# Performance work log

Hardware: AMD Instinct MI355X
Metric: run time of the kernel (lower is better)

Reference implementation:

```python
import jax, jax.numpy as jnp
import numpy as np

N = 50000
K = 4
D_IN = 256
D_OUT = 64
E = 800000

def setup_inputs() -> dict:
    key = jax.random.key(0)
    k1, k2, k3, k4, k5 = jax.random.split(key, 5)
    x = jax.random.normal(k1, (N, K, D_IN), dtype=jnp.float32)
    weight = jax.random.normal(k2, (D_IN, D_OUT), dtype=jnp.float32) * (1.0 / np.sqrt(D_IN))
    adj_rows = jax.random.randint(k3, (E,), 0, N, dtype=jnp.int32)
    adj_cols = jax.random.randint(k4, (E,), 0, N, dtype=jnp.int32)
    adj_vals = jax.random.uniform(k5, (E,), dtype=jnp.float32)
    return {"x": x, "weight": weight, "adj_rows": adj_rows, "adj_cols": adj_cols, "adj_vals": adj_vals}

def reference(x, weight, adj_rows, adj_cols, adj_vals):
    # x: [N, K, D_in]; weight: [D_in, D_out]
    # dropout p=0.0 / eval mode -> identity
    # support = x @ W for every sample k, vectorized over K
    support = jnp.einsum('nkd,df->nkf', x, weight)          # [N, K, D_out]
    # sparse adj matmul: out[r] += vals[e] * support[cols[e]]
    msgs = adj_vals[:, None, None] * support[adj_cols]       # [E, K, D_out]
    out = jax.ops.segment_sum(msgs, adj_rows, num_segments=N)  # [N, K, D_out]
    return jax.nn.relu(out)
```

## Files before the change

kernel.cpp:

```cpp
#include <hip/hip_runtime.h>
#include <hip/hip_bf16.h>
#include <stdint.h>

#define D_IN   256
#define D_OUT  64
#define KHEADS 4
#define ROWLEN 256
#define GBM    128
#define LDAB   72
#define LDWB   72
#define CAP    128

typedef __attribute__((ext_vector_type(8))) short bf16x8;
typedef __attribute__((ext_vector_type(4))) float f32x4;

__device__ __forceinline__ unsigned short f2bf(float f) {
  unsigned u = __float_as_uint(f);
  return (unsigned short)((u + 0x7fffu + ((u >> 16) & 1u)) >> 16);
}

__global__ __launch_bounds__(256) void gemm_mfma(const float* __restrict__ X,
                                                 const float* __restrict__ W,
                                                 signed char* __restrict__ Sq,
                                                 float* __restrict__ scaleArr,
                                                 int M, int Nnodes) {
  __shared__ unsigned short lA[GBM * LDAB];
  __shared__ unsigned short lWt[64 * LDWB];
  const int t    = threadIdx.x;
  const int wave = t >> 6;
  const int lane = t & 63;
  const int q    = lane >> 4;
  const int l16  = lane & 15;
  const long row0 = (long)blockIdx.x * GBM;

  f32x4 acc[2][4];
#pragma unroll
  for (int rb = 0; rb < 2; ++rb)
#pragma unroll
    for (int cb = 0; cb < 4; ++cb) acc[rb][cb] = (f32x4){0.f, 0.f, 0.f, 0.f};

  for (int k0 = 0; k0 < D_IN; k0 += 64) {
#pragma unroll
    for (int j = 0; j < 8; ++j) {
      int flat = t + j * 256;
      int r    = flat >> 4;
      int kk   = (flat & 15) << 2;
      long gr  = row0 + r;
      if (gr >= M) gr = M - 1;
      float4 v = *(const float4*)&X[gr * D_IN + k0 + kk];
      ushort4 o;
      o.x = f2bf(v.x); o.y = f2bf(v.y); o.z = f2bf(v.z); o.w = f2bf(v.w);
      *(ushort4*)&lA[r * LDAB + kk] = o;
    }
#pragma unroll
    for (int j = 0; j < 4; ++j) {
      int flat = t + j * 256;
      int kr   = flat >> 4;
      int nn   = (flat & 15) << 2;
      float4 v = *(const float4*)&W[(size_t)(k0 + kr) * D_OUT + nn];
      lWt[(nn + 0) * LDWB + kr] = f2bf(v.x);
      lWt[(nn + 1) * LDWB + kr] = f2bf(v.y);
      lWt[(nn + 2) * LDWB + kr] = f2bf(v.z);
      lWt[(nn + 3) * LDWB + kr] = f2bf(v.w);
    }
    __syncthreads();

#pragma unroll
    for (int s = 0; s < 2; ++s) {
      bf16x8 a0 = *(const bf16x8*)&lA[(wave * 32 + 0  + l16) * LDAB + s * 32 + q * 8];
      bf16x8 a1 = *(const bf16x8*)&lA[(wave * 32 + 16 + l16) * LDAB + s * 32 + q * 8];
#pragma unroll
      for (int cb = 0; cb < 4; ++cb) {
        bf16x8 b = *(const bf16x8*)&lWt[(cb * 16 + l16) * LDWB + s * 32 + q * 8];
        acc[0][cb] = __builtin_amdgcn_mfma_f32_16x16x32_bf16(a0, b, acc[0][cb], 0, 0, 0);
        acc[1][cb] = __builtin_amdgcn_mfma_f32_16x16x32_bf16(a1, b, acc[1][cb], 0, 0, 0);
      }
    }
    __syncthreads();
  }

  float nm0 = 0.f, nm1 = 0.f;
#pragma unroll
  for (int cb = 0; cb < 4; ++cb)
#pragma unroll
    for (int reg = 0; reg < 4; ++reg) {
      nm0 = fmaxf(nm0, fabsf(acc[0][cb][reg]));
      nm1 = fmaxf(nm1, fabsf(acc[1][cb][reg]));
    }
#pragma unroll
  for (int d = 1; d < 16; d <<= 1) {
    nm0 = fmaxf(nm0, __shfl_xor(nm0, d, 64));
    nm1 = fmaxf(nm1, __shfl_xor(nm1, d, 64));
  }
  const float inv0 = (nm0 > 0.f) ? 127.f / nm0 : 0.f;
  const float inv1 = (nm1 > 0.f) ? 127.f / nm1 : 0.f;
  const int node_base = blockIdx.x * 32 + wave * 8;
  if (l16 == 0) {
    int n0 = node_base + q;
    int n1 = node_base + 4 + q;
    if (n0 < Nnodes) scaleArr[n0] = nm0 / 127.f;
    if (n1 < Nnodes) scaleArr[n1] = nm1 / 127.f;
  }
#pragma unroll
  for (int rb = 0; rb < 2; ++rb) {
    const float inv = rb ? inv1 : inv0;
#pragma unroll
    for (int cb = 0; cb < 4; ++cb)
#pragma unroll
      for (int reg = 0; reg < 4; ++reg) {
        long r = row0 + wave * 32 + rb * 16 + q * 4 + reg;
        if (r < M) {
          int qi = (int)rintf(acc[rb][cb][reg] * inv);
          Sq[r * D_OUT + cb * 16 + l16] = (signed char)qi;
        }
      }
  }
}

__global__ __launch_bounds__(256) void place_kernel(const int* __restrict__ rows,
                                                    const int* __restrict__ cols,
                                                    const float* __restrict__ vals,
                                                    const float* __restrict__ scaleArr,
                                                    int* __restrict__ cnt,
                                                    uint2* __restrict__ ecv, int E) {
  int e = blockIdx.x * 256 + threadIdx.x;
  if (e < E) {
    int r = rows[e];
    int c = cols[e];
    float vp = vals[e] * scaleArr[c];
    int pos = atomicAdd(&cnt[r], 1);
    if (pos < CAP)
      ecv[((size_t)r << 7) + pos] = make_uint2((unsigned)c, __float_as_uint(vp));
  }
}

__global__ __launch_bounds__(256) void gather_kernel(const int* __restrict__ Sqi,
                                                     const int* __restrict__ cnt,
                                                     const uint2* __restrict__ ecv,
                                                     float* __restrict__ out, int n) {
  const int lane = threadIdx.x & 63;
  const int r = blockIdx.x * 4 + (threadIdx.x >> 6);
  if (r >= n) return;
  int deg = cnt[r];
  if (deg > CAP) deg = CAP;
  const uint2* __restrict__ bucket = ecv + ((size_t)r << 7);

  float4 a0 = make_float4(0.f, 0.f, 0.f, 0.f);
  float4 a1 = a0, a2 = a0, a3 = a0;
  int i = 0;
  for (; i + 4 <= deg; i += 4) {
    uint2 c0 = bucket[i], c1 = bucket[i + 1], c2 = bucket[i + 2], c3 = bucket[i + 3];
    int w0 = Sqi[(size_t)c0.x * 64 + lane];
    int w1 = Sqi[(size_t)c1.x * 64 + lane];
    int w2 = Sqi[(size_t)c2.x * 64 + lane];
    int w3 = Sqi[(size_t)c3.x * 64 + lane];
    float v0 = __uint_as_float(c0.y), v1 = __uint_as_float(c1.y);
    float v2 = __uint_as_float(c2.y), v3 = __uint_as_float(c3.y);
    a0.x += v0 * (float)(w0 << 24 >> 24); a0.y += v0 * (float)(w0 << 16 >> 24);
    a0.z += v0 * (float)(w0 <<  8 >> 24); a0.w += v0 * (float)(w0 >> 24);
    a1.x += v1 * (float)(w1 << 24 >> 24); a1.y += v1 * (float)(w1 << 16 >> 24);
    a1.z += v1 * (float)(w1 <<  8 >> 24); a1.w += v1 * (float)(w1 >> 24);
    a2.x += v2 * (float)(w2 << 24 >> 24); a2.y += v2 * (float)(w2 << 16 >> 24);
    a2.z += v2 * (float)(w2 <<  8 >> 24); a2.w += v2 * (float)(w2 >> 24);
    a3.x += v3 * (float)(w3 << 24 >> 24); a3.y += v3 * (float)(w3 << 16 >> 24);
    a3.z += v3 * (float)(w3 <<  8 >> 24); a3.w += v3 * (float)(w3 >> 24);
  }
  for (; i < deg; ++i) {
    uint2 c0 = bucket[i];
    int w0 = Sqi[(size_t)c0.x * 64 + lane];
    float v0 = __uint_as_float(c0.y);
    a0.x += v0 * (float)(w0 << 24 >> 24); a0.y += v0 * (float)(w0 << 16 >> 24);
    a0.z += v0 * (float)(w0 <<  8 >> 24); a0.w += v0 * (float)(w0 >> 24);
  }
  float4 res;
  res.x = fmaxf(a0.x + a1.x + a2.x + a3.x, 0.f);
  res.y = fmaxf(a0.y + a1.y + a2.y + a3.y, 0.f);
  res.z = fmaxf(a0.z + a1.z + a2.z + a3.z, 0.f);
  res.w = fmaxf(a0.w + a1.w + a2.w + a3.w, 0.f);
  *(float4*)&out[(size_t)r * ROWLEN + (lane << 2)] = res;
}

extern "C" void kernel_launch(void* const* d_in, const int* in_sizes, int n_in,
                              void* d_out, int out_size, void* d_ws, size_t ws_size,
                              hipStream_t stream) {
  const float* x    = (const float*)d_in[0];
  const float* w    = (const float*)d_in[1];
  const int*   rows = (const int*)d_in[2];
  const int*   cols = (const int*)d_in[3];
  const float* vals = (const float*)d_in[4];
  float* out = (float*)d_out;

  const int E = in_sizes[2];
  const int N = in_sizes[0] / (KHEADS * D_IN);
  const int M = N * KHEADS;

  char* ws = (char*)d_ws;
  size_t o = 0;
  signed char* Sq = (signed char*)(ws + o); o += (size_t)M * D_OUT;
  o = (o + 15) & ~(size_t)15;
  float* scaleArr = (float*)(ws + o); o += (size_t)N * sizeof(float);
  o = (o + 15) & ~(size_t)15;
  int* cnt = (int*)(ws + o); o += (size_t)N * sizeof(int);
  o = (o + 15) & ~(size_t)15;
  uint2* ecv = (uint2*)(ws + o);

  hipMemsetAsync(cnt, 0, (size_t)N * sizeof(int), stream);

  gemm_mfma<<<(M + GBM - 1) / GBM, 256, 0, stream>>>(x, w, Sq, scaleArr, M, N);
  place_kernel<<<(E + 255) / 256, 256, 0, stream>>>(rows, cols, vals, scaleArr, cnt, ecv, E);
  gather_kernel<<<(N + 3) / 4, 256, 0, stream>>>((const int*)Sq, cnt, ecv, out, N);
}
```

Measured before the change: 397.0 us.

## Load A fragments directly from global in GEMM and widen gather unroll

The GEMM now stages all of W into shared memory once and has each lane load its A fragments straight from global memory into registers, converting to bf16 on the fly and prefetching the next k-slice. This removes the A tile in shared memory and the per-k-step barriers. The gather kernel processes edges in groups of 8 with clamped indices and zeroed weights for the tail, which raises the number of independent loads in flight. The trade-offs are global A loads that are less coalesced (each lane reads 32 contiguous bytes from a different row) and some redundant tail loads.

```diff
diff --git a/kernel.cpp b/kernel.cpp
--- a/kernel.cpp
+++ b/kernel.cpp
@@ -7,8 +7,7 @@
 #define KHEADS 4
 #define ROWLEN 256
 #define GBM    128
-#define LDAB   72
-#define LDWB   72
+#define LDWT   264
 #define CAP    128
 
 typedef __attribute__((ext_vector_type(8))) short bf16x8;
@@ -17,6 +16,17 @@
 __device__ __forceinline__ unsigned short f2bf(float f) {
   unsigned u = __float_as_uint(f);
   return (unsigned short)((u + 0x7fffu + ((u >> 16) & 1u)) >> 16);
+}
+
+__device__ __forceinline__ bf16x8 load_a_frag(const float* __restrict__ p) {
+  float4 u = *(const float4*)p;
+  float4 v = *(const float4*)(p + 4);
+  bf16x8 r;
+  r[0] = (short)f2bf(u.x); r[1] = (short)f2bf(u.y);
+  r[2] = (short)f2bf(u.z); r[3] = (short)f2bf(u.w);
+  r[4] = (short)f2bf(v.x); r[5] = (short)f2bf(v.y);
+  r[6] = (short)f2bf(v.z); r[7] = (short)f2bf(v.w);
+  return r;
 }
 
 __global__ __launch_bounds__(256) void gemm_mfma(const float* __restrict__ X,
@@ -24,8 +34,7 @@
                                                  signed char* __restrict__ Sq,
                                                  float* __restrict__ scaleArr,
                                                  int M, int Nnodes) {
-  __shared__ unsigned short lA[GBM * LDAB];
-  __shared__ unsigned short lWt[64 * LDWB];
+  __shared__ unsigned short lWt[64 * LDWT];
   const int t    = threadIdx.x;
   const int wave = t >> 6;
   const int lane = t & 63;
@@ -33,50 +42,48 @@
   const int l16  = lane & 15;
   const long row0 = (long)blockIdx.x * GBM;
 
+#pragma unroll
+  for (int j = 0; j < 16; ++j) {
+    int flat = t + j * 256;
+    int kr   = flat >> 4;
+    int nn   = (flat & 15) << 2;
+    float4 v = *(const float4*)&W[(size_t)kr * D_OUT + nn];
+    lWt[(nn + 0) * LDWT + kr] = f2bf(v.x);
+    lWt[(nn + 1) * LDWT + kr] = f2bf(v.y);
+    lWt[(nn + 2) * LDWT + kr] = f2bf(v.z);
+    lWt[(nn + 3) * LDWT + kr] = f2bf(v.w);
+  }
+  __syncthreads();
+
+  long r0 = row0 + wave * 32 + l16;
+  long r1 = r0 + 16;
+  if (r0 >= M) r0 = M - 1;
+  if (r1 >= M) r1 = M - 1;
+  const float* px0 = X + r0 * D_IN + q * 8;
+  const float* px1 = X + r1 * D_IN + q * 8;
+
   f32x4 acc[2][4];
 #pragma unroll
   for (int rb = 0; rb < 2; ++rb)
 #pragma unroll
     for (int cb = 0; cb < 4; ++cb) acc[rb][cb] = (f32x4){0.f, 0.f, 0.f, 0.f};
 
-  for (int k0 = 0; k0 < D_IN; k0 += 64) {
-#pragma unroll
-    for (int j = 0; j < 8; ++j) {
-      int flat = t + j * 256;
-      int r    = flat >> 4;
-      int kk   = (flat & 15) << 2;
-      long gr  = row0 + r;
-      if (gr >= M) gr = M - 1;
-      float4 v = *(const float4*)&X[gr * D_IN + k0 + kk];
-      ushort4 o;
-      o.x = f2bf(v.x); o.y = f2bf(v.y); o.z = f2bf(v.z); o.w = f2bf(v.w);
-      *(ushort4*)&lA[r * LDAB + kk] = o;
-    }
-#pragma unroll
-    for (int j = 0; j < 4; ++j) {
-      int flat = t + j * 256;
-      int kr   = flat >> 4;
-      int nn   = (flat & 15) << 2;
-      float4 v = *(const float4*)&W[(size_t)(k0 + kr) * D_OUT + nn];
-      lWt[(nn + 0) * LDWB + kr] = f2bf(v.x);
-      lWt[(nn + 1) * LDWB + kr] = f2bf(v.y);
-      lWt[(nn + 2) * LDWB + kr] = f2bf(v.z);
-      lWt[(nn + 3) * LDWB + kr] = f2bf(v.w);
-    }
-    __syncthreads();
-
-#pragma unroll
-    for (int s = 0; s < 2; ++s) {
-      bf16x8 a0 = *(const bf16x8*)&lA[(wave * 32 + 0  + l16) * LDAB + s * 32 + q * 8];
-      bf16x8 a1 = *(const bf16x8*)&lA[(wave * 32 + 16 + l16) * LDAB + s * 32 + q * 8];
-#pragma unroll
-      for (int cb = 0; cb < 4; ++cb) {
-        bf16x8 b = *(const bf16x8*)&lWt[(cb * 16 + l16) * LDWB + s * 32 + q * 8];
-        acc[0][cb] = __builtin_amdgcn_mfma_f32_16x16x32_bf16(a0, b, acc[0][cb], 0, 0, 0);
-        acc[1][cb] = __builtin_amdgcn_mfma_f32_16x16x32_bf16(a1, b, acc[1][cb], 0, 0, 0);
-      }
-    }
-    __syncthreads();
+  bf16x8 a0 = load_a_frag(px0);
+  bf16x8 a1 = load_a_frag(px1);
+#pragma unroll
+  for (int s = 0; s < 8; ++s) {
+    bf16x8 na0, na1;
+    if (s < 7) {
+      na0 = load_a_frag(px0 + (s + 1) * 32);
+      na1 = load_a_frag(px1 + (s + 1) * 32);
+    }
+#pragma unroll
+    for (int cb = 0; cb < 4; ++cb) {
+      bf16x8 b = *(const bf16x8*)&lWt[(cb * 16 + l16) * LDWT + s * 32 + q * 8];
+      acc[0][cb] = __builtin_amdgcn_mfma_f32_16x16x32_bf16(a0, b, acc[0][cb], 0, 0, 0);
+      acc[1][cb] = __builtin_amdgcn_mfma_f32_16x16x32_bf16(a1, b, acc[1][cb], 0, 0, 0);
+    }
+    a0 = na0; a1 = na1;
   }
 
   float nm0 = 0.f, nm1 = 0.f;
@@ -145,38 +152,41 @@
   if (deg > CAP) deg = CAP;
   const uint2* __restrict__ bucket = ecv + ((size_t)r << 7);
 
-  float4 a0 = make_float4(0.f, 0.f, 0.f, 0.f);
-  float4 a1 = a0, a2 = a0, a3 = a0;
-  int i = 0;
-  for (; i + 4 <= deg; i += 4) {
-    uint2 c0 = bucket[i], c1 = bucket[i + 1], c2 = bucket[i + 2], c3 = bucket[i + 3];
-    int w0 = Sqi[(size_t)c0.x * 64 + lane];
-    int w1 = Sqi[(size_t)c1.x * 64 + lane];
-    int w2 = Sqi[(size_t)c2.x * 64 + lane];
-    int w3 = Sqi[(size_t)c3.x * 64 + lane];
-    float v0 = __uint_as_float(c0.y), v1 = __uint_as_float(c1.y);
-    float v2 = __uint_as_float(c2.y), v3 = __uint_as_float(c3.y);
-    a0.x += v0 * (float)(w0 << 24 >> 24); a0.y += v0 * (float)(w0 << 16 >> 24);
-    a0.z += v0 * (float)(w0 <<  8 >> 24); a0.w += v0 * (float)(w0 >> 24);
-    a1.x += v1 * (float)(w1 << 24 >> 24); a1.y += v1 * (float)(w1 << 16 >> 24);
-    a1.z += v1 * (float)(w1 <<  8 >> 24); a1.w += v1 * (float)(w1 >> 24);
-    a2.x += v2 * (float)(w2 << 24 >> 24); a2.y += v2 * (float)(w2 << 16 >> 24);
-    a2.z += v2 * (float)(w2 <<  8 >> 24); a2.w += v2 * (float)(w2 >> 24);
-    a3.x += v3 * (float)(w3 << 24 >> 24); a3.y += v3 * (float)(w3 << 16 >> 24);
-    a3.z += v3 * (float)(w3 <<  8 >> 24); a3.w += v3 * (float)(w3 >> 24);
-  }
-  for (; i < deg; ++i) {
-    uint2 c0 = bucket[i];
-    int w0 = Sqi[(size_t)c0.x * 64 + lane];
-    float v0 = __uint_as_float(c0.y);
-    a0.x += v0 * (float)(w0 << 24 >> 24); a0.y += v0 * (float)(w0 << 16 >> 24);
-    a0.z += v0 * (float)(w0 <<  8 >> 24); a0.w += v0 * (float)(w0 >> 24);
+  float4 acc[8];
+#pragma unroll
+  for (int j = 0; j < 8; ++j) acc[j] = make_float4(0.f, 0.f, 0.f, 0.f);
+
+  for (int i = 0; i < deg; i += 8) {
+    const int lim = deg - 1;
+    unsigned col[8];
+    float    val[8];
+#pragma unroll
+    for (int j = 0; j < 8; ++j) {
+      int idx = i + j;
+      uint2 e = bucket[idx <= lim ? idx : lim];
+      col[j] = e.x;
+      val[j] = (idx <= lim) ? __uint_as_float(e.y) : 0.f;
+    }
+    int wv[8];
+#pragma unroll
+    for (int j = 0; j < 8; ++j) wv[j] = Sqi[(size_t)col[j] * 64 + lane];
+#pragma unroll
+    for (int j = 0; j < 8; ++j) {
+      acc[j].x += val[j] * (float)(wv[j] << 24 >> 24);
+      acc[j].y += val[j] * (float)(wv[j] << 16 >> 24);
+      acc[j].z += val[j] * (float)(wv[j] <<  8 >> 24);
+      acc[j].w += val[j] * (float)(wv[j] >> 24);
+    }
   }
   float4 res;
-  res.x = fmaxf(a0.x + a1.x + a2.x + a3.x, 0.f);
-  res.y = fmaxf(a0.y + a1.y + a2.y + a3.y, 0.f);
-  res.z = fmaxf(a0.z + a1.z + a2.z + a3.z, 0.f);
-  res.w = fmaxf(a0.w + a1.w + a2.w + a3.w, 0.f);
+  res.x = fmaxf(acc[0].x + acc[1].x + acc[2].x + acc[3].x +
+                acc[4].x + acc[5].x + acc[6].x + acc[7].x, 0.f);
+  res.y = fmaxf(acc[0].y + acc[1].y + acc[2].y + acc[3].y +
+                acc[4].y + acc[5].y + acc[6].y + acc[7].y, 0.f);
+  res.z = fmaxf(acc[0].z + acc[1].z + acc[2].z + acc[3].z +
+                acc[4].z + acc[5].z + acc[6].z + acc[7].z, 0.f);
+  res.w = fmaxf(acc[0].w + acc[1].w + acc[2].w + acc[3].w +
+                acc[4].w + acc[5].w + acc[6].w + acc[7].w, 0.f);
   *(float4*)&out[(size_t)r * ROWLEN + (lane << 2)] = res;
 }
 
```

Result: no change. 404.7 us (+1.9%).
